# Kernel optimization log

Hardware: AMD Instinct MI355X
Metric: run time of the kernel (lower is better)

The kernel has to match this reference:

```python
import jax, jax.numpy as jnp
import numpy as np

B, T, D, H = 4, 2048, 1024, 16
HD = D // H

def setup_inputs() -> dict:
    key = jax.random.key(0)
    ks = jax.random.split(key, 7)
    s = 1.0 / np.sqrt(D)
    return {
        "x": jax.random.normal(ks[0], (B, T, D), dtype=jnp.float32),
        "w_qkv": jax.random.uniform(ks[1], (D, 3 * D), jnp.float32, -s, s),
        "b_qkv": jax.random.uniform(ks[2], (3 * D,), jnp.float32, -s, s),
        "w_proj": jax.random.uniform(ks[3], (D, D), jnp.float32, -s, s),
        "b_proj": jax.random.uniform(ks[4], (D,), jnp.float32, -s, s),
        "ln_gamma": jnp.ones((D,), jnp.float32),
        "ln_beta": jnp.zeros((D,), jnp.float32),
    }

def reference(x, w_qkv, b_qkv, w_proj, b_proj, ln_gamma, ln_beta):
    eps = 1e-5
    scale = HD ** -0.5
    residual = x
    # Pre-norm LayerNorm over last dim
    mu = jnp.mean(x, axis=-1, keepdims=True)
    var = jnp.mean(jnp.square(x - mu), axis=-1, keepdims=True)
    xn = (x - mu) * jax.lax.rsqrt(var + eps) * ln_gamma + ln_beta
    # QKV projection: (B,T,3D) -> (3,B,H,T,HD)
    qkv = xn @ w_qkv + b_qkv
    qkv = qkv.reshape(B, T, 3, H, HD).transpose(2, 0, 3, 1, 4)
    q, k, v = qkv[0], qkv[1], qkv[2]
    # Scaled dot-product attention (full T x T scores, as in source)
    attn = jnp.einsum('bhqd,bhkd->bhqk', q, k) * scale
    attn = jax.nn.softmax(attn, axis=-1)
    out = jnp.einsum('bhqk,bhkd->bhqd', attn, v)
    out = out.transpose(0, 2, 1, 3).reshape(B, T, D)
    out = out @ w_proj + b_proj
    return residual + out
```

## Files before the change

### kernel.cpp

```cpp
#include <hip/hip_runtime.h>
#include <cstdint>
#include <cstddef>

#define B_ 4
#define T_ 2048
#define D_ 1024
#define H_ 16

typedef __attribute__((ext_vector_type(8))) short short8;
typedef __attribute__((ext_vector_type(4))) float f32x4;
typedef __attribute__((ext_vector_type(8))) unsigned short u16x8;

__device__ __forceinline__ unsigned short f2b16(float f) {
  union { float f; unsigned int u; } un; un.f = f;
  unsigned int r = un.u + 0x7fffu + ((un.u >> 16) & 1u);
  return (unsigned short)(r >> 16);
}
__device__ __forceinline__ void async_cp16(const void* g, void* l) {
  __builtin_amdgcn_global_load_lds((const __attribute__((address_space(1))) void*)g,
                                   (__attribute__((address_space(3))) void*)l,
                                   16, 0, 0);
}

__global__ __launch_bounds__(256) void ln_kernel(const float* __restrict__ x,
                                                 const float* __restrict__ gamma,
                                                 const float* __restrict__ beta,
                                                 unsigned short* __restrict__ xn) {
  const int row = blockIdx.x;
  const int t = threadIdx.x;
  const float4 v = ((const float4*)(x + (size_t)row * D_))[t];
  float s  = v.x + v.y + v.z + v.w;
  float s2 = v.x*v.x + v.y*v.y + v.z*v.z + v.w*v.w;
  #pragma unroll
  for (int off = 32; off > 0; off >>= 1) {
    s  += __shfl_down(s, off);
    s2 += __shfl_down(s2, off);
  }
  __shared__ float sh[8];
  const int wv = t >> 6, lane = t & 63;
  if (lane == 0) { sh[wv] = s; sh[4 + wv] = s2; }
  __syncthreads();
  if (t == 0) {
    float ts  = sh[0] + sh[1] + sh[2] + sh[3];
    float ts2 = sh[4] + sh[5] + sh[6] + sh[7];
    float mu  = ts * (1.0f / D_);
    float var = ts2 * (1.0f / D_) - mu * mu;
    sh[0] = mu;
    sh[1] = rsqrtf(var + 1e-5f);
  }
  __syncthreads();
  const float mu = sh[0], rs = sh[1];
  const float4 g  = ((const float4*)gamma)[t];
  const float4 bb = ((const float4*)beta)[t];
  ushort4 o;
  o.x = f2b16((v.x - mu) * rs * g.x + bb.x);
  o.y = f2b16((v.y - mu) * rs * g.y + bb.y);
  o.z = f2b16((v.z - mu) * rs * g.z + bb.z);
  o.w = f2b16((v.w - mu) * rs * g.w + bb.w);
  ((ushort4*)(xn + (size_t)row * D_))[t] = o;
}

__global__ __launch_bounds__(256) void transpose_cast(const float* __restrict__ w,
                                                      unsigned short* __restrict__ wT,
                                                      int K, int N) {
  __shared__ float tile[32][33];
  const int n0 = blockIdx.x * 32;
  const int k0 = blockIdx.y * 32;
  const int tx = threadIdx.x, ty = threadIdx.y;
  #pragma unroll
  for (int i = 0; i < 32; i += 8)
    tile[ty + i][tx] = w[(size_t)(k0 + ty + i) * N + n0 + tx];
  __syncthreads();
  #pragma unroll
  for (int i = 0; i < 32; i += 8)
    wT[(size_t)(n0 + ty + i) * K + k0 + tx] = f2b16(tile[tx][ty + i]);
}

__global__ __launch_bounds__(256) void transpose_v(const unsigned short* __restrict__ vB,
                                                   unsigned short* __restrict__ vtB) {
  __shared__ unsigned short tile[64 * 66];
  const int tid = threadIdx.x;
  const int bh = blockIdx.x;
  const int t0 = blockIdx.y * 64;
  const int lr = tid >> 2, lc = (tid & 3) * 16;
  const unsigned short* src = vB + ((size_t)bh * T_ + t0) * 64;
  *(u16x8*)&tile[lr * 66 + lc]     = *(const u16x8*)(src + (size_t)lr * 64 + lc);
  *(u16x8*)&tile[lr * 66 + lc + 8] = *(const u16x8*)(src + (size_t)lr * 64 + lc + 8);
  __syncthreads();
  const int dv = tid >> 2, cb = (tid & 3) * 16;
  unsigned short outv[16];
  #pragma unroll
  for (int j = 0; j < 16; ++j) {
    const int c = cb + j;
    const int t = ((c >> 1) & 1) * 32 + (c & 1) * 16 + (c >> 2);
    outv[j] = tile[t * 66 + dv];
  }
  unsigned short* dst = vtB + ((size_t)bh * 64 + dv) * T_ + t0 + cb;
  *(u16x8*)dst       = *(const u16x8*)&outv[0];
  *(u16x8*)(dst + 8) = *(const u16x8*)&outv[8];
}

template <int MODE>
__global__ __launch_bounds__(256) void gemm_bt(const unsigned short* __restrict__ A,
                                               const unsigned short* __restrict__ Bt,
                                               const float* __restrict__ bias,
                                               const float* __restrict__ resid,
                                               unsigned short* __restrict__ qB,
                                               unsigned short* __restrict__ kB,
                                               unsigned short* __restrict__ vB,
                                               float* __restrict__ outF,
                                               int M, int N, int K) {
  __shared__ unsigned short As[128 * 32];
  __shared__ unsigned short Bs[128 * 32];
  const int tid  = threadIdx.x;
  const int lane = tid & 63;
  const int wv   = tid >> 6;
  const int wm   = (wv & 1) * 64;
  const int wn   = (wv >> 1) * 64;
  const int tileM = blockIdx.x * 128;
  const int tileN = blockIdx.y * 128;
  const int l15 = lane & 15, quad = lane >> 4;
  const int sRow = tid >> 2;
  const int sCol = (tid & 3) * 8;

  f32x4 acc[4][4] = {};

  const unsigned short* aG0 = A  + (size_t)(tileM + sRow) * K + sCol;
  const unsigned short* aG1 = A  + (size_t)(tileM + 64 + sRow) * K + sCol;
  const unsigned short* bG0 = Bt + (size_t)(tileN + sRow) * K + sCol;
  const unsigned short* bG1 = Bt + (size_t)(tileN + 64 + sRow) * K + sCol;
  unsigned short* lA0 = &As[tid * 8];
  unsigned short* lA1 = &As[2048 + tid * 8];
  unsigned short* lB0 = &Bs[tid * 8];
  unsigned short* lB1 = &Bs[2048 + tid * 8];

  for (int k0 = 0; k0 < K; k0 += 32) {
    async_cp16(aG0 + k0, lA0);
    async_cp16(aG1 + k0, lA1);
    async_cp16(bG0 + k0, lB0);
    async_cp16(bG1 + k0, lB1);
    __syncthreads();

    short8 a[4], b[4];
    #pragma unroll
    for (int i = 0; i < 4; ++i) {
      a[i] = *(const short8*)&As[(wm + i * 16 + l15) * 32 + quad * 8];
      b[i] = *(const short8*)&Bs[(wn + i * 16 + l15) * 32 + quad * 8];
    }
    #pragma unroll
    for (int mi = 0; mi < 4; ++mi)
      #pragma unroll
      for (int ni = 0; ni < 4; ++ni)
        acc[mi][ni] = __builtin_amdgcn_mfma_f32_16x16x32_bf16(a[mi], b[ni], acc[mi][ni], 0, 0, 0);
    __syncthreads();
  }

  if constexpr (MODE == 1) {
    #pragma unroll
    for (int ni = 0; ni < 4; ++ni) {
      const int col = tileN + wn + ni * 16 + l15;
      const float bv = bias[col];
      #pragma unroll
      for (int mi = 0; mi < 4; ++mi) {
        #pragma unroll
        for (int r = 0; r < 4; ++r) {
          const int row = tileM + wm + mi * 16 + quad * 4 + r;
          const size_t idx = (size_t)row * N + col;
          outF[idx] = acc[mi][ni][r] + bv + resid[idx];
        }
      }
    }
  } else {
    __shared__ unsigned short Es[4][64 * 72];
    unsigned short* E = Es[wv];
    const int colBase = tileN + wn;
    #pragma unroll
    for (int ni = 0; ni < 4; ++ni) {
      const int col = colBase + ni * 16 + l15;
      const float bv = bias[col];
      const float sc = (col < 1024) ? 0.180336880f : 1.0f;
      #pragma unroll
      for (int mi = 0; mi < 4; ++mi)
        #pragma unroll
        for (int r = 0; r < 4; ++r)
          E[(mi * 16 + quad * 4 + r) * 72 + ni * 16 + l15] =
              f2b16((acc[mi][ni][r] + bv) * sc);
    }
    const int sec = colBase >> 10;
    const int hh  = (colBase & 1023) >> 6;
    unsigned short* outSec = (sec == 0) ? qB : (sec == 1) ? kB : vB;
    #pragma unroll
    for (int it = 0; it < 8; ++it) {
      const int lrow = it * 8 + (lane >> 3);
      const int row = tileM + wm + lrow;
      const int b_ = row >> 11, t = row & 2047;
      const u16x8 val = *(const u16x8*)&E[lrow * 72 + (lane & 7) * 8];
      *(u16x8*)(outSec + ((size_t)(b_ * 16 + hh) * T_ + t) * 64 + (lane & 7) * 8) = val;
    }
  }
}

__global__ __launch_bounds__(256, 3) void attn_mfma(const unsigned short* __restrict__ qB,
                                                    const unsigned short* __restrict__ kB,
                                                    const unsigned short* __restrict__ vtB,
                                                    unsigned short* __restrict__ aout) {
  __shared__ unsigned short Ks[2][64 * 64];
  __shared__ unsigned short Vs[2][64 * 64];
  __shared__ unsigned short Pw[4][32 * 72];

  const int tid = threadIdx.x;
  const int bid = blockIdx.x;
  const int bh = bid & 63;
  const int qb = bid >> 6;
  const int b = bh >> 4, h = bh & 15;
  const int wv = tid >> 6, lane = tid & 63;
  const int l15 = lane & 15, quad = lane >> 4;

  const unsigned short* qP = qB  + (size_t)bh * T_ * 64;
  const unsigned short* kP = kB  + (size_t)bh * T_ * 64;
  const unsigned short* vP = vtB + (size_t)bh * 64 * T_;
  const int q0 = qb * 128 + wv * 32;

  short8 qf[2][2];
  #pragma unroll
  for (int mi = 0; mi < 2; ++mi)
    #pragma unroll
    for (int ks = 0; ks < 2; ++ks)
      qf[mi][ks] = *(const short8*)(qP + ((size_t)(q0 + mi * 16 + l15)) * 64 + ks * 32 + quad * 8);

  const short8 onesf = {0x3F80, 0x3F80, 0x3F80, 0x3F80, 0x3F80, 0x3F80, 0x3F80, 0x3F80};
  f32x4 accO[2][5] = {};

  const int lrow  = lane >> 3;
  const int lchnk = (lane & 7) ^ (lrow & 7);
  const size_t kOff0 = (size_t)((wv * 2 + 0) * 8 + lrow) * 64 + lchnk * 8;
  const size_t kOff1 = (size_t)((wv * 2 + 1) * 8 + lrow) * 64 + lchnk * 8;
  const size_t vOff0 = (size_t)((wv * 2 + 0) * 8 + lrow) * T_ + lchnk * 8;
  const size_t vOff1 = (size_t)((wv * 2 + 1) * 8 + lrow) * T_ + lchnk * 8;
  const int lOff0 = (wv * 2 + 0) * 512 + lane * 8;
  const int lOff1 = (wv * 2 + 1) * 512 + lane * 8;

  async_cp16(kP + kOff0, &Ks[0][lOff0]);
  async_cp16(kP + kOff1, &Ks[0][lOff1]);
  async_cp16(vP + vOff0, &Vs[0][lOff0]);
  async_cp16(vP + vOff1, &Vs[0][lOff1]);
  __syncthreads();

  for (int kt = 0; kt < 32; ++kt) {
    const int buf = kt & 1;
    if (kt + 1 < 32) {
      const unsigned short* kg = kP + (size_t)(kt + 1) * 64 * 64;
      const unsigned short* vg = vP + (kt + 1) * 64;
      async_cp16(kg + kOff0, &Ks[buf ^ 1][lOff0]);
      async_cp16(kg + kOff1, &Ks[buf ^ 1][lOff1]);
      async_cp16(vg + vOff0, &Vs[buf ^ 1][lOff0]);
      async_cp16(vg + vOff1, &Vs[buf ^ 1][lOff1]);
    }
    const unsigned short* K_ = Ks[buf];
    const unsigned short* V_ = Vs[buf];
    unsigned short* P = Pw[wv];

    f32x4 accS[2][4] = {};
    #pragma unroll
    for (int ks = 0; ks < 2; ++ks) {
      #pragma unroll
      for (int c = 0; c < 4; ++c) {
        const short8 kb = *(const short8*)&K_[(c * 16 + l15) * 64 +
                                              (((ks << 2) | quad) ^ (l15 & 7)) * 8];
        accS[0][c] = __builtin_amdgcn_mfma_f32_16x16x32_bf16(qf[0][ks], kb, accS[0][c], 0, 0, 0);
        accS[1][c] = __builtin_amdgcn_mfma_f32_16x16x32_bf16(qf[1][ks], kb, accS[1][c], 0, 0, 0);
      }
    }

    #pragma unroll
    for (int mi = 0; mi < 2; ++mi) {
      #pragma unroll
      for (int r = 0; r < 4; ++r) {
        ushort4 pv;
        union { float f; unsigned int u; } e;
        e.f = __builtin_amdgcn_exp2f(accS[mi][0][r]); pv.x = (unsigned short)(e.u >> 16);
        e.f = __builtin_amdgcn_exp2f(accS[mi][1][r]); pv.y = (unsigned short)(e.u >> 16);
        e.f = __builtin_amdgcn_exp2f(accS[mi][2][r]); pv.z = (unsigned short)(e.u >> 16);
        e.f = __builtin_amdgcn_exp2f(accS[mi][3][r]); pv.w = (unsigned short)(e.u >> 16);
        *(ushort4*)&P[(mi * 16 + quad * 4 + r) * 72 + 4 * l15] = pv;
      }
    }

    #pragma unroll
    for (int ks = 0; ks < 2; ++ks) {
      short8 vb[4], pa[2];
      #pragma unroll
      for (int nj = 0; nj < 4; ++nj)
        vb[nj] = *(const short8*)&V_[(nj * 16 + l15) * 64 +
                                     (((ks << 2) | quad) ^ (l15 & 7)) * 8];
      #pragma unroll
      for (int mi = 0; mi < 2; ++mi)
        pa[mi] = *(const short8*)&P[(mi * 16 + l15) * 72 + ks * 32 + quad * 8];
      #pragma unroll
      for (int mi = 0; mi < 2; ++mi) {
        #pragma unroll
        for (int nj = 0; nj < 4; ++nj)
          accO[mi][nj] = __builtin_amdgcn_mfma_f32_16x16x32_bf16(pa[mi], vb[nj], accO[mi][nj], 0, 0, 0);
        accO[mi][4] = __builtin_amdgcn_mfma_f32_16x16x32_bf16(pa[mi], onesf, accO[mi][4], 0, 0, 0);
      }
    }

    __syncthreads();
  }

  #pragma unroll
  for (int mi = 0; mi < 2; ++mi) {
    #pragma unroll
    for (int r = 0; r < 4; ++r) {
      const float inv = 1.0f / accO[mi][4][r];
      const int row = q0 + mi * 16 + quad * 4 + r;
      unsigned short* op = aout + (size_t)(b * T_ + row) * D_ + h * 64 + l15;
      #pragma unroll
      for (int nj = 0; nj < 4; ++nj)
        op[nj * 16] = f2b16(accO[mi][nj][r] * inv);
    }
  }
}

extern "C" void kernel_launch(void* const* d_in, const int* in_sizes, int n_in,
                              void* d_out, int out_size, void* d_ws, size_t ws_size,
                              hipStream_t stream) {
  const float* x      = (const float*)d_in[0];
  const float* w_qkv  = (const float*)d_in[1];
  const float* b_qkv  = (const float*)d_in[2];
  const float* w_proj = (const float*)d_in[3];
  const float* b_proj = (const float*)d_in[4];
  const float* ln_g   = (const float*)d_in[5];
  const float* ln_b   = (const float*)d_in[6];
  float* out = (float*)d_out;

  char* ws = (char*)d_ws;
  unsigned short* xn   = (unsigned short*)(ws);
  unsigned short* wTq  = (unsigned short*)(ws + (size_t)(16 << 20));
  unsigned short* wTp  = (unsigned short*)(ws + (size_t)(22 << 20));
  unsigned short* qBuf = (unsigned short*)(ws + (size_t)(24 << 20));
  unsigned short* kBuf = (unsigned short*)(ws + (size_t)(40 << 20));
  unsigned short* vBuf = (unsigned short*)(ws + (size_t)(56 << 20));
  unsigned short* vtB  = (unsigned short*)(ws + (size_t)(72 << 20));
  unsigned short* aout = xn;

  ln_kernel<<<8192, 256, 0, stream>>>(x, ln_g, ln_b, xn);
  transpose_cast<<<dim3(96, 32), dim3(32, 8), 0, stream>>>(w_qkv, wTq, 1024, 3072);
  transpose_cast<<<dim3(32, 32), dim3(32, 8), 0, stream>>>(w_proj, wTp, 1024, 1024);
  gemm_bt<0><<<dim3(64, 24), 256, 0, stream>>>(xn, wTq, b_qkv, nullptr,
                                               qBuf, kBuf, vBuf, nullptr, 8192, 3072, 1024);
  transpose_v<<<dim3(64, 32), 256, 0, stream>>>(vBuf, vtB);
  attn_mfma<<<1024, 256, 0, stream>>>(qBuf, kBuf, vtB, aout);
  gemm_bt<1><<<dim3(64, 8), 256, 0, stream>>>(aout, wTp, b_proj, x,
                                              nullptr, nullptr, nullptr, out, 8192, 1024, 1024);
}
```

Measured before the change: 303.9 us.

## Keep softmax probabilities in registers via transposed QK MFMA, drop LDS staging

```diff
diff --git a/kernel.cpp b/kernel.cpp
--- a/kernel.cpp
+++ b/kernel.cpp
@@ -92,7 +92,7 @@
   #pragma unroll
   for (int j = 0; j < 16; ++j) {
     const int c = cb + j;
-    const int t = ((c >> 1) & 1) * 32 + (c & 1) * 16 + (c >> 2);
+    const int t = (c & 32) | ((c & 4) << 2) | ((c & 16) >> 1) | ((c & 8) >> 1) | (c & 3);
     outv[j] = tile[t * 66 + dv];
   }
   unsigned short* dst = vtB + ((size_t)bh * 64 + dv) * T_ + t0 + cb;
@@ -200,13 +200,12 @@
   }
 }
 
-__global__ __launch_bounds__(256, 3) void attn_mfma(const unsigned short* __restrict__ qB,
+__global__ __launch_bounds__(256, 4) void attn_mfma(const unsigned short* __restrict__ qB,
                                                     const unsigned short* __restrict__ kB,
                                                     const unsigned short* __restrict__ vtB,
                                                     unsigned short* __restrict__ aout) {
   __shared__ unsigned short Ks[2][64 * 64];
   __shared__ unsigned short Vs[2][64 * 64];
-  __shared__ unsigned short Pw[4][32 * 72];
 
   const int tid = threadIdx.x;
   const int bid = blockIdx.x;
@@ -258,50 +257,50 @@
     }
     const unsigned short* K_ = Ks[buf];
     const unsigned short* V_ = Vs[buf];
-    unsigned short* P = Pw[wv];
-
-    f32x4 accS[2][4] = {};
+
+    f32x4 accT[4][2] = {};
     #pragma unroll
     for (int ks = 0; ks < 2; ++ks) {
       #pragma unroll
-      for (int c = 0; c < 4; ++c) {
-        const short8 kb = *(const short8*)&K_[(c * 16 + l15) * 64 +
+      for (int cc = 0; cc < 4; ++cc) {
+        const short8 kb = *(const short8*)&K_[(cc * 16 + l15) * 64 +
                                               (((ks << 2) | quad) ^ (l15 & 7)) * 8];
-        accS[0][c] = __builtin_amdgcn_mfma_f32_16x16x32_bf16(qf[0][ks], kb, accS[0][c], 0, 0, 0);
-        accS[1][c] = __builtin_amdgcn_mfma_f32_16x16x32_bf16(qf[1][ks], kb, accS[1][c], 0, 0, 0);
+        accT[cc][0] = __builtin_amdgcn_mfma_f32_16x16x32_bf16(kb, qf[0][ks], accT[cc][0], 0, 0, 0);
+        accT[cc][1] = __builtin_amdgcn_mfma_f32_16x16x32_bf16(kb, qf[1][ks], accT[cc][1], 0, 0, 0);
       }
     }
 
+    short8 pa[2][2];
     #pragma unroll
     for (int mi = 0; mi < 2; ++mi) {
       #pragma unroll
-      for (int r = 0; r < 4; ++r) {
-        ushort4 pv;
-        union { float f; unsigned int u; } e;
-        e.f = __builtin_amdgcn_exp2f(accS[mi][0][r]); pv.x = (unsigned short)(e.u >> 16);
-        e.f = __builtin_amdgcn_exp2f(accS[mi][1][r]); pv.y = (unsigned short)(e.u >> 16);
-        e.f = __builtin_amdgcn_exp2f(accS[mi][2][r]); pv.z = (unsigned short)(e.u >> 16);
-        e.f = __builtin_amdgcn_exp2f(accS[mi][3][r]); pv.w = (unsigned short)(e.u >> 16);
-        *(ushort4*)&P[(mi * 16 + quad * 4 + r) * 72 + 4 * l15] = pv;
+      for (int ks = 0; ks < 2; ++ks) {
+        union { unsigned short u[8]; short8 s; } pk;
+        #pragma unroll
+        for (int r = 0; r < 4; ++r) {
+          union { float f; unsigned int u; } e0, e1;
+          e0.f = __builtin_amdgcn_exp2f(accT[2 * ks + 0][mi][r]);
+          e1.f = __builtin_amdgcn_exp2f(accT[2 * ks + 1][mi][r]);
+          pk.u[r]     = (unsigned short)(e0.u >> 16);
+          pk.u[4 + r] = (unsigned short)(e1.u >> 16);
+        }
+        pa[mi][ks] = pk.s;
       }
     }
 
     #pragma unroll
     for (int ks = 0; ks < 2; ++ks) {
-      short8 vb[4], pa[2];
+      short8 vb[4];
       #pragma unroll
       for (int nj = 0; nj < 4; ++nj)
         vb[nj] = *(const short8*)&V_[(nj * 16 + l15) * 64 +
                                      (((ks << 2) | quad) ^ (l15 & 7)) * 8];
       #pragma unroll
-      for (int mi = 0; mi < 2; ++mi)
-        pa[mi] = *(const short8*)&P[(mi * 16 + l15) * 72 + ks * 32 + quad * 8];
-      #pragma unroll
       for (int mi = 0; mi < 2; ++mi) {
         #pragma unroll
         for (int nj = 0; nj < 4; ++nj)
-          accO[mi][nj] = __builtin_amdgcn_mfma_f32_16x16x32_bf16(pa[mi], vb[nj], accO[mi][nj], 0, 0, 0);
-        accO[mi][4] = __builtin_amdgcn_mfma_f32_16x16x32_bf16(pa[mi], onesf, accO[mi][4], 0, 0, 0);
+          accO[mi][nj] = __builtin_amdgcn_mfma_f32_16x16x32_bf16(pa[mi][ks], vb[nj], accO[mi][nj], 0, 0, 0);
+        accO[mi][4] = __builtin_amdgcn_mfma_f32_16x16x32_bf16(pa[mi][ks], onesf, accO[mi][4], 0, 0, 0);
       }
     }
 
```

Result: faster. 279.6 us (-8.0%).
